# Performance work log

Hardware: AMD Instinct MI355X
Metric: run time of the kernel (lower is better)

The kernel has to match this reference:

```python
import jax, jax.numpy as jnp
import numpy as np

B, S, H = 1, 1024, 2048
I = 1408            # moe_intermediate_size
E = 16              # n_routed_experts
TOP_K = 4           # num_experts_per_tok
N_GROUP = 4
TOPK_GROUP = 2
N_SHARED = 2
SCALE = 2.5         # routed_scaling_factor
SI = I * N_SHARED   # shared expert intermediate size


def setup_inputs() -> dict:
    key = jax.random.key(0)
    ks = jax.random.split(key, 9)
    s = 0.02
    return {
        "hidden_states": jax.random.normal(ks[0], (B, S, H), jnp.float32),
        "gate_w": jax.random.normal(ks[1], (E, H), jnp.float32) * s,
        "gate_bias": jnp.zeros((E,), jnp.float32),
        "w_gate": jax.random.normal(ks[2], (E, I, H), jnp.float32) * s,
        "w_up": jax.random.normal(ks[3], (E, I, H), jnp.float32) * s,
        "w_down": jax.random.normal(ks[4], (E, H, I), jnp.float32) * s,
        "sw_gate": jax.random.normal(ks[5], (SI, H), jnp.float32) * s,
        "sw_up": jax.random.normal(ks[6], (SI, H), jnp.float32) * s,
        "sw_down": jax.random.normal(ks[7], (H, SI), jnp.float32) * s,
    }


def _gate(x, gate_w, gate_bias):
    # x: [T, H] -> combine weights [T, E]
    T = x.shape[0]
    logits = x @ gate_w.T                                  # [T, E]
    scores = jax.nn.sigmoid(logits) + gate_bias            # [T, E]
    gsz = E // N_GROUP
    group_scores = scores.reshape(T, N_GROUP, gsz).max(-1)  # [T, G]
    _, sel_groups = jax.lax.top_k(group_scores, TOPK_GROUP)  # [T, kg]
    gmask = jnp.zeros((T, N_GROUP), scores.dtype).at[
        jnp.arange(T)[:, None], sel_groups].set(1.0)        # [T, G]
    mask = jnp.repeat(gmask, gsz, axis=1)                   # [T, E]
    masked = scores * mask
    w, idx = jax.lax.top_k(masked, TOP_K)                   # [T, k]
    w = w / (w.sum(-1, keepdims=True) + 1e-6)
    combine = jnp.zeros((T, E), w.dtype).at[
        jnp.arange(T)[:, None], idx].add(w)                 # [T, E]
    return combine


def reference(hidden_states, gate_w, gate_bias, w_gate, w_up, w_down,
              sw_gate, sw_up, sw_down):
    x = hidden_states.reshape(-1, H)                        # [T, H]
    combine = _gate(x, gate_w, gate_bias)                   # [T, E]
    # dense dispatch: every expert sees all tokens; zero combine weight
    # for unrouted tokens reproduces the masked gather/scatter loop exactly
    g = jnp.einsum('th,eih->tei', x, w_gate)
    u = jnp.einsum('th,eih->tei', x, w_up)
    h = jax.nn.silu(g) * u                                   # [T, E, I]
    y = jnp.einsum('tei,ehi->teh', h, w_down)                # [T, E, H]
    routed = jnp.einsum('te,teh->th', combine, y) * SCALE    # [T, H]
    # shared experts (one wide MLP)
    shared = (jax.nn.silu(x @ sw_gate.T) * (x @ sw_up.T)) @ sw_down.T
    return (routed + shared).reshape(B, S, H)
```

## Files before the change

### kernel.cpp

```cpp
#include <hip/hip_runtime.h>
#include <hip/hip_bf16.h>

#define TTOK  1024
#define HDIM  2048
#define IDIM  1408
#define NEXP  16
#define SIDIM 2816
#define RSCALE 2.5f

typedef __bf16 bf16_t;
typedef bf16_t bf16x8 __attribute__((ext_vector_type(8)));
typedef float  f32x4  __attribute__((ext_vector_type(4)));

static const size_t OFF_XBF   = 0;
static const size_t OFF_HBUF  = 4194304;
static const size_t OFF_SHBUF = OFF_HBUF + 17301504;
static const size_t OFF_TOPKI = OFF_SHBUF + 5767168;
static const size_t OFF_TOPKW = OFF_TOPKI + 16384;
static const size_t OFF_TOKL  = OFF_TOPKW + 16384;
static const size_t OFF_WGTL  = OFF_TOKL + 24576;
static const size_t OFF_CNT   = OFF_WGTL + 24576;
static const size_t OFF_POFF  = OFF_CNT + 256;

union Pack4 { bf16_t b[4]; unsigned long long u64; };

__device__ __forceinline__ f32x4 mfma16(bf16x8 a, bf16x8 b, f32x4 c) {
    return __builtin_amdgcn_mfma_f32_16x16x32_bf16(a, b, c, 0, 0, 0);
}
__device__ __forceinline__ bf16x8 frag_read(const bf16_t* lds, int row, int slot) {
    int sw = slot ^ (row & 7);
    return *(const bf16x8*)(lds + row * 64 + sw * 8);
}

__global__ __launch_bounds__(256) void k_convert(const float* __restrict__ x,
                                                 bf16_t* __restrict__ xb, int n) {
    int i = (blockIdx.x * 256 + threadIdx.x) * 4;
    if (i < n) {
        float4 v = *(const float4*)(x + i);
        Pack4 p;
        p.b[0] = (bf16_t)v.x; p.b[1] = (bf16_t)v.y;
        p.b[2] = (bf16_t)v.z; p.b[3] = (bf16_t)v.w;
        *(unsigned long long*)(xb + i) = p.u64;
    }
}

__global__ __launch_bounds__(256) void k_gate(const float* __restrict__ x,
                                              const float* __restrict__ gw,
                                              const float* __restrict__ gb,
                                              int* __restrict__ topki,
                                              float* __restrict__ topkw,
                                              int* __restrict__ counts) {
    int t = blockIdx.x;
    int tid = threadIdx.x;
    int e = tid >> 4, li = tid & 15;
    const float* xr = x + (size_t)t * HDIM;
    const float* wr = gw + (size_t)e * HDIM;
    float s = 0.f;
#pragma unroll
    for (int j = 0; j < 32; ++j) {
        int off = (j * 16 + li) * 4;
        float4 a = *(const float4*)(xr + off);
        float4 b = *(const float4*)(wr + off);
        s += a.x * b.x + a.y * b.y + a.z * b.z + a.w * b.w;
    }
    __shared__ float red[16][16];
    __shared__ float scores[16];
    red[e][li] = s;
    __syncthreads();
    if (tid < 16) {
        float acc = 0.f;
#pragma unroll
        for (int j = 0; j < 16; ++j) acc += red[tid][j];
        scores[tid] = 1.f / (1.f + expf(-acc)) + gb[tid];
    }
    __syncthreads();
    if (tid == 0) {
        float gsc[4];
#pragma unroll
        for (int g = 0; g < 4; ++g) {
            float m = scores[g * 4];
            for (int j = 1; j < 4; ++j) m = fmaxf(m, scores[g * 4 + j]);
            gsc[g] = m;
        }
        bool gsel[4] = {false, false, false, false};
        for (int k = 0; k < 2; ++k) {
            int best = 0; float bv = -1e30f;
            for (int g = 0; g < 4; ++g)
                if (!gsel[g] && gsc[g] > bv) { bv = gsc[g]; best = g; }
            gsel[best] = true;
        }
        float msc[16];
        for (int i = 0; i < 16; ++i) msc[i] = gsel[i >> 2] ? scores[i] : -1.f;
        int bidx[4]; float bw[4]; float wsum = 0.f;
        for (int k = 0; k < 4; ++k) {
            int best = 0; float bv = -2e30f;
            for (int i = 0; i < 16; ++i)
                if (msc[i] > bv) { bv = msc[i]; best = i; }
            msc[best] = -3e30f;
            bidx[k] = best; bw[k] = bv; wsum += bv;
        }
        float inv = 1.f / (wsum + 1e-6f);
        for (int k = 0; k < 4; ++k) {
            topki[t * 4 + k] = bidx[k];
            topkw[t * 4 + k] = bw[k] * inv * RSCALE;
            atomicAdd(&counts[bidx[k]], 1);
        }
    }
}

__global__ void k_scan(const int* __restrict__ counts, int* __restrict__ poff) {
    if (threadIdx.x == 0 && blockIdx.x == 0) {
        int acc = 0;
        for (int e = 0; e < NEXP; ++e) {
            poff[e] = acc;
            acc += (counts[e] + 127) & ~127;
        }
    }
}

__global__ __launch_bounds__(64) void k_compact(const int* __restrict__ topki,
                                                const float* __restrict__ topkw,
                                                const int* __restrict__ counts,
                                                const int* __restrict__ poff,
                                                int* __restrict__ tokl,
                                                float* __restrict__ wgtl) {
    int e = blockIdx.x;
    int lane = threadIdx.x;
    int base = poff[e];
    int cur = 0;
    for (int t0 = 0; t0 < TTOK; t0 += 64) {
        int t = t0 + lane;
        int4   idx = *(const int4*)(topki + t * 4);
        float4 wv  = *(const float4*)(topkw + t * 4);
        bool has = false; float w = 0.f;
        if      (idx.x == e) { has = true; w = wv.x; }
        else if (idx.y == e) { has = true; w = wv.y; }
        else if (idx.z == e) { has = true; w = wv.z; }
        else if (idx.w == e) { has = true; w = wv.w; }
        unsigned long long b = __ballot(has);
        int pos = cur + __popcll(b & ((1ull << lane) - 1ull));
        if (has) { tokl[base + pos] = t; wgtl[base + pos] = w; }
        cur += __popcll(b);
    }
    int padded = (counts[e] + 127) & ~127;
    for (int i = cur + lane; i < padded; i += 64) {
        tokl[base + i] = -1; wgtl[base + i] = 0.f;
    }
}

__global__ __launch_bounds__(256, 2) void k_mlp1_routed(
        const bf16_t* __restrict__ xb, const float* __restrict__ wg,
        const float* __restrict__ wu, const int* __restrict__ counts,
        const int* __restrict__ poff, const int* __restrict__ tokl,
        bf16_t* __restrict__ hbuf) {
    int bid = blockIdx.x;
    int e = bid / 88, rem = bid % 88;
    int mt = rem / 11, nt = rem % 11;
    int cnt = counts[e];
    if (mt * 128 >= cnt) return;
    int rowbase = poff[e] + mt * 128;
    const float* wgp = wg + (size_t)e * IDIM * HDIM + (size_t)(nt * 128) * HDIM;
    const float* wup = wu + (size_t)e * IDIM * HDIM + (size_t)(nt * 128) * HDIM;

    __shared__ bf16_t aL[128 * 64];
    __shared__ bf16_t gL[128 * 64];
    __shared__ bf16_t uL[128 * 64];

    int tid = threadIdx.x;
    int lane = tid & 63;
    int wid = tid >> 6;
    int wm = wid >> 1, wn = wid & 1;

    f32x4 accg[4][4], accu[4][4];
#pragma unroll
    for (int m = 0; m < 4; ++m)
#pragma unroll
        for (int n = 0; n < 4; ++n) {
            accg[m][n] = (f32x4){0.f, 0.f, 0.f, 0.f};
            accu[m][n] = (f32x4){0.f, 0.f, 0.f, 0.f};
        }

    int arow_ = tid >> 3, alane = tid & 7;
    int brow_ = tid >> 4, blane = tid & 15;
    int atok[4];
#pragma unroll
    for (int p = 0; p < 4; ++p) atok[p] = tokl[rowbase + p * 32 + arow_];

    for (int kt = 0; kt < HDIM / 64; ++kt) {
#pragma unroll
        for (int p = 0; p < 4; ++p) {
            int r = p * 32 + arow_;
            uint4 v = make_uint4(0, 0, 0, 0);
            int tok = atok[p];
            if (tok >= 0)
                v = *(const uint4*)(xb + (size_t)tok * HDIM + kt * 64 + alane * 8);
            int sw = alane ^ (r & 7);
            *(uint4*)(aL + r * 64 + sw * 8) = v;
        }
#pragma unroll
        for (int p = 0; p < 8; ++p) {
            int r = p * 16 + brow_;
            const float* sg = wgp + (size_t)r * HDIM + kt * 64 + blane * 4;
            const float* su = wup + (size_t)r * HDIM + kt * 64 + blane * 4;
            float4 vg = *(const float4*)sg;
            float4 vu = *(const float4*)su;
            int sw = (blane >> 1) ^ (r & 7);
            int half = blane & 1;
            Pack4 pg, pu;
            pg.b[0] = (bf16_t)vg.x; pg.b[1] = (bf16_t)vg.y;
            pg.b[2] = (bf16_t)vg.z; pg.b[3] = (bf16_t)vg.w;
            pu.b[0] = (bf16_t)vu.x; pu.b[1] = (bf16_t)vu.y;
            pu.b[2] = (bf16_t)vu.z; pu.b[3] = (bf16_t)vu.w;
            *(unsigned long long*)(gL + r * 64 + sw * 8 + half * 4) = pg.u64;
            *(unsigned long long*)(uL + r * 64 + sw * 8 + half * 4) = pu.u64;
        }
        __syncthreads();
#pragma unroll
        for (int ks = 0; ks < 2; ++ks) {
            bf16x8 af[4], bg[4], bu[4];
            int slot = ks * 4 + (lane >> 4);
#pragma unroll
            for (int m = 0; m < 4; ++m)
                af[m] = frag_read(aL, wm * 64 + m * 16 + (lane & 15), slot);
#pragma unroll
            for (int n = 0; n < 4; ++n) {
                bg[n] = frag_read(gL, wn * 64 + n * 16 + (lane & 15), slot);
                bu[n] = frag_read(uL, wn * 64 + n * 16 + (lane & 15), slot);
            }
#pragma unroll
            for (int m = 0; m < 4; ++m)
#pragma unroll
                for (int n = 0; n < 4; ++n) {
                    accg[m][n] = mfma16(af[m], bg[n], accg[m][n]);
                    accu[m][n] = mfma16(af[m], bu[n], accu[m][n]);
                }
        }
        __syncthreads();
    }
    int col0 = nt * 128 + wn * 64 + (lane & 15);
#pragma unroll
    for (int m = 0; m < 4; ++m) {
        int rloc = wm * 64 + m * 16 + ((lane >> 4) << 2);
#pragma unroll
        for (int ri = 0; ri < 4; ++ri) {
            bf16_t* dst = hbuf + (size_t)(rowbase + rloc + ri) * IDIM + col0;
#pragma unroll
            for (int n = 0; n < 4; ++n) {
                float g = accg[m][n][ri], u = accu[m][n][ri];
                float h = g / (1.f + __expf(-g)) * u;
                dst[n * 16] = (bf16_t)h;
            }
        }
    }
}

__global__ __launch_bounds__(256, 2) void k_mlp1_shared(
        const bf16_t* __restrict__ xb, const float* __restrict__ swg,
        const float* __restrict__ swu, bf16_t* __restrict__ shbuf) {
    int bid = blockIdx.x;
    int mt = bid / 22, nt = bid % 22;
    int rowbase = mt * 128;
    const float* wgp = swg + (size_t)(nt * 128) * HDIM;
    const float* wup = swu + (size_t)(nt * 128) * HDIM;

    __shared__ bf16_t aL[128 * 64];
    __shared__ bf16_t gL[128 * 64];
    __shared__ bf16_t uL[128 * 64];

    int tid = threadIdx.x;
    int lane = tid & 63;
    int wid = tid >> 6;
    int wm = wid >> 1, wn = wid & 1;

    f32x4 accg[4][4], accu[4][4];
#pragma unroll
    for (int m = 0; m < 4; ++m)
#pragma unroll
        for (int n = 0; n < 4; ++n) {
            accg[m][n] = (f32x4){0.f, 0.f, 0.f, 0.f};
            accu[m][n] = (f32x4){0.f, 0.f, 0.f, 0.f};
        }
    int arow_ = tid >> 3, alane = tid & 7;
    int brow_ = tid >> 4, blane = tid & 15;

    for (int kt = 0; kt < HDIM / 64; ++kt) {
#pragma unroll
        for (int p = 0; p < 4; ++p) {
            int r = p * 32 + arow_;
            uint4 v = *(const uint4*)(xb + (size_t)(rowbase + r) * HDIM + kt * 64 + alane * 8);
            int sw = alane ^ (r & 7);
            *(uint4*)(aL + r * 64 + sw * 8) = v;
        }
#pragma unroll
        for (int p = 0; p < 8; ++p) {
            int r = p * 16 + brow_;
            float4 vg = *(const float4*)(wgp + (size_t)r * HDIM + kt * 64 + blane * 4);
            float4 vu = *(const float4*)(wup + (size_t)r * HDIM + kt * 64 + blane * 4);
            int sw = (blane >> 1) ^ (r & 7);
            int half = blane & 1;
            Pack4 pg, pu;
            pg.b[0] = (bf16_t)vg.x; pg.b[1] = (bf16_t)vg.y;
            pg.b[2] = (bf16_t)vg.z; pg.b[3] = (bf16_t)vg.w;
            pu.b[0] = (bf16_t)vu.x; pu.b[1] = (bf16_t)vu.y;
            pu.b[2] = (bf16_t)vu.z; pu.b[3] = (bf16_t)vu.w;
            *(unsigned long long*)(gL + r * 64 + sw * 8 + half * 4) = pg.u64;
            *(unsigned long long*)(uL + r * 64 + sw * 8 + half * 4) = pu.u64;
        }
        __syncthreads();
#pragma unroll
        for (int ks = 0; ks < 2; ++ks) {
            bf16x8 af[4], bg[4], bu[4];
            int slot = ks * 4 + (lane >> 4);
#pragma unroll
            for (int m = 0; m < 4; ++m)
                af[m] = frag_read(aL, wm * 64 + m * 16 + (lane & 15), slot);
#pragma unroll
            for (int n = 0; n < 4; ++n) {
                bg[n] = frag_read(gL, wn * 64 + n * 16 + (lane & 15), slot);
                bu[n] = frag_read(uL, wn * 64 + n * 16 + (lane & 15), slot);
            }
#pragma unroll
            for (int m = 0; m < 4; ++m)
#pragma unroll
                for (int n = 0; n < 4; ++n) {
                    accg[m][n] = mfma16(af[m], bg[n], accg[m][n]);
                    accu[m][n] = mfma16(af[m], bu[n], accu[m][n]);
                }
        }
        __syncthreads();
    }
    int col0 = nt * 128 + wn * 64 + (lane & 15);
#pragma unroll
    for (int m = 0; m < 4; ++m) {
        int rloc = wm * 64 + m * 16 + ((lane >> 4) << 2);
#pragma unroll
        for (int ri = 0; ri < 4; ++ri) {
            bf16_t* dst = shbuf + (size_t)(rowbase + rloc + ri) * SIDIM + col0;
#pragma unroll
            for (int n = 0; n < 4; ++n) {
                float g = accg[m][n][ri], u = accu[m][n][ri];
                float h = g / (1.f + __expf(-g)) * u;
                dst[n * 16] = (bf16_t)h;
            }
        }
    }
}

__global__ __launch_bounds__(256, 2) void k_down_shared(
        const bf16_t* __restrict__ shbuf, const float* __restrict__ swd,
        float* __restrict__ out) {
    int bid = blockIdx.x;
    int mt = bid >> 4, nt = bid & 15;
    int rowbase = mt * 128;
    const float* wp = swd + (size_t)(nt * 128) * SIDIM;

    __shared__ bf16_t aL[128 * 64];
    __shared__ bf16_t bL[128 * 64];

    int tid = threadIdx.x;
    int lane = tid & 63;
    int wid = tid >> 6;
    int wm = wid >> 1, wn = wid & 1;

    f32x4 acc[4][4];
#pragma unroll
    for (int m = 0; m < 4; ++m)
#pragma unroll
        for (int n = 0; n < 4; ++n) acc[m][n] = (f32x4){0.f, 0.f, 0.f, 0.f};

    int arow_ = tid >> 3, alane = tid & 7;
    int brow_ = tid >> 4, blane = tid & 15;

    for (int kt = 0; kt < SIDIM / 64; ++kt) {
#pragma unroll
        for (int p = 0; p < 4; ++p) {
            int r = p * 32 + arow_;
            uint4 v = *(const uint4*)(shbuf + (size_t)(rowbase + r) * SIDIM + kt * 64 + alane * 8);
            int sw = alane ^ (r & 7);
            *(uint4*)(aL + r * 64 + sw * 8) = v;
        }
#pragma unroll
        for (int p = 0; p < 8; ++p) {
            int r = p * 16 + brow_;
            float4 v = *(const float4*)(wp + (size_t)r * SIDIM + kt * 64 + blane * 4);
            int sw = (blane >> 1) ^ (r & 7);
            int half = blane & 1;
            Pack4 pb;
            pb.b[0] = (bf16_t)v.x; pb.b[1] = (bf16_t)v.y;
            pb.b[2] = (bf16_t)v.z; pb.b[3] = (bf16_t)v.w;
            *(unsigned long long*)(bL + r * 64 + sw * 8 + half * 4) = pb.u64;
        }
        __syncthreads();
#pragma unroll
        for (int ks = 0; ks < 2; ++ks) {
            bf16x8 af[4], bf[4];
            int slot = ks * 4 + (lane >> 4);
#pragma unroll
            for (int m = 0; m < 4; ++m)
                af[m] = frag_read(aL, wm * 64 + m * 16 + (lane & 15), slot);
#pragma unroll
            for (int n = 0; n < 4; ++n)
                bf[n] = frag_read(bL, wn * 64 + n * 16 + (lane & 15), slot);
#pragma unroll
            for (int m = 0; m < 4; ++m)
#pragma unroll
                for (int n = 0; n < 4; ++n)
                    acc[m][n] = mfma16(af[m], bf[n], acc[m][n]);
        }
        __syncthreads();
    }
    int col0 = nt * 128 + wn * 64 + (lane & 15);
#pragma unroll
    for (int m = 0; m < 4; ++m) {
        int rloc = wm * 64 + m * 16 + ((lane >> 4) << 2);
#pragma unroll
        for (int ri = 0; ri < 4; ++ri) {
            float* dst = out + (size_t)(rowbase + rloc + ri) * HDIM + col0;
#pragma unroll
            for (int n = 0; n < 4; ++n) dst[n * 16] = acc[m][n][ri];
        }
    }
}

__global__ __launch_bounds__(256, 2) void k_down_routed(
        const bf16_t* __restrict__ hbuf, const float* __restrict__ wd,
        const int* __restrict__ counts, const int* __restrict__ poff,
        const int* __restrict__ tokl, const float* __restrict__ wgtl,
        float* __restrict__ out) {
    int bid = blockIdx.x;
    int e = bid >> 7, rem = bid & 127;
    int mt = rem >> 4, nt = rem & 15;
    int cnt = counts[e];
    if (mt * 128 >= cnt) return;
    int rowbase = poff[e] + mt * 128;
    const float* wp = wd + (size_t)e * HDIM * IDIM + (size_t)(nt * 128) * IDIM;

    __shared__ bf16_t aL[128 * 64];
    __shared__ bf16_t bL[128 * 64];

    int tid = threadIdx.x;
    int lane = tid & 63;
    int wid = tid >> 6;
    int wm = wid >> 1, wn = wid & 1;

    f32x4 acc[4][4];
#pragma unroll
    for (int m = 0; m < 4; ++m)
#pragma unroll
        for (int n = 0; n < 4; ++n) acc[m][n] = (f32x4){0.f, 0.f, 0.f, 0.f};

    int arow_ = tid >> 3, alane = tid & 7;
    int brow_ = tid >> 4, blane = tid & 15;

    for (int kt = 0; kt < IDIM / 64; ++kt) {
#pragma unroll
        for (int p = 0; p < 4; ++p) {
            int r = p * 32 + arow_;
            uint4 v = *(const uint4*)(hbuf + (size_t)(rowbase + r) * IDIM + kt * 64 + alane * 8);
            int sw = alane ^ (r & 7);
            *(uint4*)(aL + r * 64 + sw * 8) = v;
        }
#pragma unroll
        for (int p = 0; p < 8; ++p) {
            int r = p * 16 + brow_;
            float4 v = *(const float4*)(wp + (size_t)r * IDIM + kt * 64 + blane * 4);
            int sw = (blane >> 1) ^ (r & 7);
            int half = blane & 1;
            Pack4 pb;
            pb.b[0] = (bf16_t)v.x; pb.b[1] = (bf16_t)v.y;
            pb.b[2] = (bf16_t)v.z; pb.b[3] = (bf16_t)v.w;
            *(unsigned long long*)(bL + r * 64 + sw * 8 + half * 4) = pb.u64;
        }
        __syncthreads();
#pragma unroll
        for (int ks = 0; ks < 2; ++ks) {
            bf16x8 af[4], bf[4];
            int slot = ks * 4 + (lane >> 4);
#pragma unroll
            for (int m = 0; m < 4; ++m)
                af[m] = frag_read(aL, wm * 64 + m * 16 + (lane & 15), slot);
#pragma unroll
            for (int n = 0; n < 4; ++n)
                bf[n] = frag_read(bL, wn * 64 + n * 16 + (lane & 15), slot);
#pragma unroll
            for (int m = 0; m < 4; ++m)
#pragma unroll
                for (int n = 0; n < 4; ++n)
                    acc[m][n] = mfma16(af[m], bf[n], acc[m][n]);
        }
        __syncthreads();
    }
    int col0 = nt * 128 + wn * 64 + (lane & 15);
#pragma unroll
    for (int m = 0; m < 4; ++m) {
        int rloc = wm * 64 + m * 16 + ((lane >> 4) << 2);
#pragma unroll
        for (int ri = 0; ri < 4; ++ri) {
            int row = rowbase + rloc + ri;
            int tok = tokl[row];
            if (tok < 0) continue;
            float wgt = wgtl[row];
            float* dst = out + (size_t)tok * HDIM + col0;
#pragma unroll
            for (int n = 0; n < 4; ++n)
                atomicAdd(dst + n * 16, wgt * acc[m][n][ri]);
        }
    }
}

extern "C" void kernel_launch(void* const* d_in, const int* in_sizes, int n_in,
                              void* d_out, int out_size, void* d_ws, size_t ws_size,
                              hipStream_t stream) {
    const float* x       = (const float*)d_in[0];
    const float* gate_w  = (const float*)d_in[1];
    const float* gate_b  = (const float*)d_in[2];
    const float* w_gate  = (const float*)d_in[3];
    const float* w_up    = (const float*)d_in[4];
    const float* w_down  = (const float*)d_in[5];
    const float* sw_gate = (const float*)d_in[6];
    const float* sw_up   = (const float*)d_in[7];
    const float* sw_down = (const float*)d_in[8];
    float* out = (float*)d_out;

    char* ws = (char*)d_ws;
    bf16_t* xb    = (bf16_t*)(ws + OFF_XBF);
    bf16_t* hbuf  = (bf16_t*)(ws + OFF_HBUF);
    bf16_t* shbuf = (bf16_t*)(ws + OFF_SHBUF);
    int*    topki = (int*)(ws + OFF_TOPKI);
    float*  topkw = (float*)(ws + OFF_TOPKW);
    int*    tokl  = (int*)(ws + OFF_TOKL);
    float*  wgtl  = (float*)(ws + OFF_WGTL);
    int*    counts= (int*)(ws + OFF_CNT);
    int*    poff  = (int*)(ws + OFF_POFF);

    hipMemsetAsync(counts, 0, 64, stream);
    k_convert<<<2048, 256, 0, stream>>>(x, xb, TTOK * HDIM);
    k_gate<<<TTOK, 256, 0, stream>>>(x, gate_w, gate_b, topki, topkw, counts);
    k_scan<<<1, 64, 0, stream>>>(counts, poff);
    k_compact<<<NEXP, 64, 0, stream>>>(topki, topkw, counts, poff, tokl, wgtl);
    k_mlp1_routed<<<NEXP * 8 * 11, 256, 0, stream>>>(xb, w_gate, w_up, counts, poff, tokl, hbuf);
    k_mlp1_shared<<<8 * 22, 256, 0, stream>>>(xb, sw_gate, sw_up, shbuf);
    k_down_shared<<<8 * 16, 256, 0, stream>>>(shbuf, sw_down, out);
    k_down_routed<<<NEXP * 8 * 16, 256, 0, stream>>>(hbuf, w_down, counts, poff, tokl, wgtl, out);
}
```

Measured before the change: 0.9997 ms.

## Merge routed/shared MLP kernels, halve N tile, prefetch next K tile, swizzle XCDs

Routed and shared expert GEMMs are merged into one launch for the up/gate stage and one for the down stage. The N tile shrinks from 128 to 64, which doubles the block count and lowers register and LDS use, so occupancy can be raised to 3 blocks per CU in the down kernel. Global loads for the next K tile are issued into registers before the MFMA loop (register double-buffering), and a block-index swizzle groups neighbouring tiles onto the same XCD to improve L2 reuse. The shared down projection now uses atomics into a zeroed output, which adds a memset, and narrower tiles re-read the activations more often.

```diff
diff --git a/kernel.cpp b/kernel.cpp
--- a/kernel.cpp
+++ b/kernel.cpp
@@ -30,6 +30,10 @@
 __device__ __forceinline__ bf16x8 frag_read(const bf16_t* lds, int row, int slot) {
     int sw = slot ^ (row & 7);
     return *(const bf16x8*)(lds + row * 64 + sw * 8);
+}
+__device__ __forceinline__ int xcd_swz(int bid, int grid) {
+    int q = grid >> 3;
+    return (bid & 7) * q + (bid >> 3);
 }
 
 __global__ __launch_bounds__(256) void k_convert(const float* __restrict__ x,
@@ -148,104 +152,134 @@
     }
 }
 
-__global__ __launch_bounds__(256, 2) void k_mlp1_routed(
-        const bf16_t* __restrict__ xb, const float* __restrict__ wg,
-        const float* __restrict__ wu, const int* __restrict__ counts,
-        const int* __restrict__ poff, const int* __restrict__ tokl,
-        bf16_t* __restrict__ hbuf) {
-    int bid = blockIdx.x;
-    int e = bid / 88, rem = bid % 88;
-    int mt = rem / 11, nt = rem % 11;
-    int cnt = counts[e];
-    if (mt * 128 >= cnt) return;
-    int rowbase = poff[e] + mt * 128;
-    const float* wgp = wg + (size_t)e * IDIM * HDIM + (size_t)(nt * 128) * HDIM;
-    const float* wup = wu + (size_t)e * IDIM * HDIM + (size_t)(nt * 128) * HDIM;
+#define GRID_MLP1 (NEXP * 22 * 8 + 44 * 8)
+
+__global__ __launch_bounds__(256, 2) void k_mlp1(
+        const bf16_t* __restrict__ xb,
+        const float* __restrict__ wg, const float* __restrict__ wu,
+        const float* __restrict__ swg, const float* __restrict__ swu,
+        const int* __restrict__ counts, const int* __restrict__ poff,
+        const int* __restrict__ tokl,
+        bf16_t* __restrict__ hbuf, bf16_t* __restrict__ shbuf) {
+    int bid = xcd_swz(blockIdx.x, GRID_MLP1);
+    bool routed = bid < NEXP * 22 * 8;
+    const float *wgp, *wup;
+    bf16_t* outp;
+    int old_, rowbase, ntcol;
+    if (routed) {
+        int e = bid / 176, rem = bid % 176;
+        int nt = rem / 8, mt = rem % 8;
+        if (mt * 128 >= counts[e]) return;
+        rowbase = poff[e] + mt * 128;
+        size_t wo = (size_t)e * IDIM * HDIM + (size_t)(nt * 64) * HDIM;
+        wgp = wg + wo; wup = wu + wo;
+        outp = hbuf; old_ = IDIM; ntcol = nt * 64;
+    } else {
+        int sb = bid - NEXP * 22 * 8;
+        int nt = sb / 8, mt = sb % 8;
+        rowbase = mt * 128;
+        size_t wo = (size_t)(nt * 64) * HDIM;
+        wgp = swg + wo; wup = swu + wo;
+        outp = shbuf; old_ = SIDIM; ntcol = nt * 64;
+    }
 
     __shared__ bf16_t aL[128 * 64];
-    __shared__ bf16_t gL[128 * 64];
-    __shared__ bf16_t uL[128 * 64];
-
-    int tid = threadIdx.x;
-    int lane = tid & 63;
-    int wid = tid >> 6;
+    __shared__ bf16_t gL[64 * 64];
+    __shared__ bf16_t uL[64 * 64];
+
+    int tid = threadIdx.x, lane = tid & 63, wid = tid >> 6;
     int wm = wid >> 1, wn = wid & 1;
-
-    f32x4 accg[4][4], accu[4][4];
+    int arow_ = tid >> 3, alane = tid & 7;
+    int brow_ = tid >> 4, blane = tid & 15;
+
+    int tokA[4];
+#pragma unroll
+    for (int p = 0; p < 4; ++p) {
+        int r = rowbase + p * 32 + arow_;
+        int tk = routed ? tokl[r] : r;
+        tokA[p] = tk < 0 ? 0 : tk;
+    }
+
+    f32x4 accg[4][2], accu[4][2];
 #pragma unroll
     for (int m = 0; m < 4; ++m)
 #pragma unroll
-        for (int n = 0; n < 4; ++n) {
+        for (int n = 0; n < 2; ++n) {
             accg[m][n] = (f32x4){0.f, 0.f, 0.f, 0.f};
             accu[m][n] = (f32x4){0.f, 0.f, 0.f, 0.f};
         }
 
-    int arow_ = tid >> 3, alane = tid & 7;
-    int brow_ = tid >> 4, blane = tid & 15;
-    int atok[4];
-#pragma unroll
-    for (int p = 0; p < 4; ++p) atok[p] = tokl[rowbase + p * 32 + arow_];
+    uint4  sa[4];
+    float4 sg[4], su[4];
+
+#define MLP1_LOAD(KT) do {                                                        \
+    _Pragma("unroll")                                                             \
+    for (int p = 0; p < 4; ++p)                                                   \
+        sa[p] = *(const uint4*)(xb + (size_t)tokA[p] * HDIM + (KT) * 64 + alane * 8); \
+    _Pragma("unroll")                                                             \
+    for (int p = 0; p < 4; ++p) {                                                 \
+        size_t off = (size_t)(p * 16 + brow_) * HDIM + (KT) * 64 + blane * 4;     \
+        sg[p] = *(const float4*)(wgp + off);                                      \
+        su[p] = *(const float4*)(wup + off);                                      \
+    }                                                                             \
+} while (0)
+
+    MLP1_LOAD(0);
 
     for (int kt = 0; kt < HDIM / 64; ++kt) {
 #pragma unroll
         for (int p = 0; p < 4; ++p) {
             int r = p * 32 + arow_;
-            uint4 v = make_uint4(0, 0, 0, 0);
-            int tok = atok[p];
-            if (tok >= 0)
-                v = *(const uint4*)(xb + (size_t)tok * HDIM + kt * 64 + alane * 8);
-            int sw = alane ^ (r & 7);
-            *(uint4*)(aL + r * 64 + sw * 8) = v;
-        }
-#pragma unroll
-        for (int p = 0; p < 8; ++p) {
+            *(uint4*)(aL + r * 64 + (alane ^ (r & 7)) * 8) = sa[p];
+        }
+#pragma unroll
+        for (int p = 0; p < 4; ++p) {
             int r = p * 16 + brow_;
-            const float* sg = wgp + (size_t)r * HDIM + kt * 64 + blane * 4;
-            const float* su = wup + (size_t)r * HDIM + kt * 64 + blane * 4;
-            float4 vg = *(const float4*)sg;
-            float4 vu = *(const float4*)su;
-            int sw = (blane >> 1) ^ (r & 7);
-            int half = blane & 1;
+            int sw = (blane >> 1) ^ (r & 7), half = blane & 1;
             Pack4 pg, pu;
-            pg.b[0] = (bf16_t)vg.x; pg.b[1] = (bf16_t)vg.y;
-            pg.b[2] = (bf16_t)vg.z; pg.b[3] = (bf16_t)vg.w;
-            pu.b[0] = (bf16_t)vu.x; pu.b[1] = (bf16_t)vu.y;
-            pu.b[2] = (bf16_t)vu.z; pu.b[3] = (bf16_t)vu.w;
+            pg.b[0] = (bf16_t)sg[p].x; pg.b[1] = (bf16_t)sg[p].y;
+            pg.b[2] = (bf16_t)sg[p].z; pg.b[3] = (bf16_t)sg[p].w;
+            pu.b[0] = (bf16_t)su[p].x; pu.b[1] = (bf16_t)su[p].y;
+            pu.b[2] = (bf16_t)su[p].z; pu.b[3] = (bf16_t)su[p].w;
             *(unsigned long long*)(gL + r * 64 + sw * 8 + half * 4) = pg.u64;
             *(unsigned long long*)(uL + r * 64 + sw * 8 + half * 4) = pu.u64;
         }
         __syncthreads();
+        int ktn = (kt + 1 < HDIM / 64) ? kt + 1 : kt;
+        MLP1_LOAD(ktn);
 #pragma unroll
         for (int ks = 0; ks < 2; ++ks) {
-            bf16x8 af[4], bg[4], bu[4];
+            bf16x8 af[4], bg[2], bu[2];
             int slot = ks * 4 + (lane >> 4);
 #pragma unroll
             for (int m = 0; m < 4; ++m)
                 af[m] = frag_read(aL, wm * 64 + m * 16 + (lane & 15), slot);
 #pragma unroll
-            for (int n = 0; n < 4; ++n) {
-                bg[n] = frag_read(gL, wn * 64 + n * 16 + (lane & 15), slot);
-                bu[n] = frag_read(uL, wn * 64 + n * 16 + (lane & 15), slot);
+            for (int n = 0; n < 2; ++n) {
+                bg[n] = frag_read(gL, wn * 32 + n * 16 + (lane & 15), slot);
+                bu[n] = frag_read(uL, wn * 32 + n * 16 + (lane & 15), slot);
             }
 #pragma unroll
             for (int m = 0; m < 4; ++m)
 #pragma unroll
-                for (int n = 0; n < 4; ++n) {
+                for (int n = 0; n < 2; ++n) {
                     accg[m][n] = mfma16(af[m], bg[n], accg[m][n]);
                     accu[m][n] = mfma16(af[m], bu[n], accu[m][n]);
                 }
         }
         __syncthreads();
     }
-    int col0 = nt * 128 + wn * 64 + (lane & 15);
+#undef MLP1_LOAD
+
+    int col0 = ntcol + wn * 32 + (lane & 15);
 #pragma unroll
     for (int m = 0; m < 4; ++m) {
         int rloc = wm * 64 + m * 16 + ((lane >> 4) << 2);
 #pragma unroll
         for (int ri = 0; ri < 4; ++ri) {
-            bf16_t* dst = hbuf + (size_t)(rowbase + rloc + ri) * IDIM + col0;
-#pragma unroll
-            for (int n = 0; n < 4; ++n) {
+            bf16_t* dst = outp + (size_t)(rowbase + rloc + ri) * old_ + col0;
+#pragma unroll
+            for (int n = 0; n < 2; ++n) {
                 float g = accg[m][n][ri], u = accu[m][n][ri];
                 float h = g / (1.f + __expf(-g)) * u;
                 dst[n * 16] = (bf16_t)h;
@@ -254,255 +288,124 @@
     }
 }
 
-__global__ __launch_bounds__(256, 2) void k_mlp1_shared(
-        const bf16_t* __restrict__ xb, const float* __restrict__ swg,
-        const float* __restrict__ swu, bf16_t* __restrict__ shbuf) {
-    int bid = blockIdx.x;
-    int mt = bid / 22, nt = bid % 22;
-    int rowbase = mt * 128;
-    const float* wgp = swg + (size_t)(nt * 128) * HDIM;
-    const float* wup = swu + (size_t)(nt * 128) * HDIM;
-
-    __shared__ bf16_t aL[128 * 64];
-    __shared__ bf16_t gL[128 * 64];
-    __shared__ bf16_t uL[128 * 64];
-
-    int tid = threadIdx.x;
-    int lane = tid & 63;
-    int wid = tid >> 6;
-    int wm = wid >> 1, wn = wid & 1;
-
-    f32x4 accg[4][4], accu[4][4];
-#pragma unroll
-    for (int m = 0; m < 4; ++m)
-#pragma unroll
-        for (int n = 0; n < 4; ++n) {
-            accg[m][n] = (f32x4){0.f, 0.f, 0.f, 0.f};
-            accu[m][n] = (f32x4){0.f, 0.f, 0.f, 0.f};
-        }
-    int arow_ = tid >> 3, alane = tid & 7;
-    int brow_ = tid >> 4, blane = tid & 15;
-
-    for (int kt = 0; kt < HDIM / 64; ++kt) {
-#pragma unroll
-        for (int p = 0; p < 4; ++p) {
-            int r = p * 32 + arow_;
-            uint4 v = *(const uint4*)(xb + (size_t)(rowbase + r) * HDIM + kt * 64 + alane * 8);
-            int sw = alane ^ (r & 7);
-            *(uint4*)(aL + r * 64 + sw * 8) = v;
-        }
-#pragma unroll
-        for (int p = 0; p < 8; ++p) {
-            int r = p * 16 + brow_;
-            float4 vg = *(const float4*)(wgp + (size_t)r * HDIM + kt * 64 + blane * 4);
-            float4 vu = *(const float4*)(wup + (size_t)r * HDIM + kt * 64 + blane * 4);
-            int sw = (blane >> 1) ^ (r & 7);
-            int half = blane & 1;
-            Pack4 pg, pu;
-            pg.b[0] = (bf16_t)vg.x; pg.b[1] = (bf16_t)vg.y;
-            pg.b[2] = (bf16_t)vg.z; pg.b[3] = (bf16_t)vg.w;
-            pu.b[0] = (bf16_t)vu.x; pu.b[1] = (bf16_t)vu.y;
-            pu.b[2] = (bf16_t)vu.z; pu.b[3] = (bf16_t)vu.w;
-            *(unsigned long long*)(gL + r * 64 + sw * 8 + half * 4) = pg.u64;
-            *(unsigned long long*)(uL + r * 64 + sw * 8 + half * 4) = pu.u64;
-        }
-        __syncthreads();
-#pragma unroll
-        for (int ks = 0; ks < 2; ++ks) {
-            bf16x8 af[4], bg[4], bu[4];
-            int slot = ks * 4 + (lane >> 4);
-#pragma unroll
-            for (int m = 0; m < 4; ++m)
-                af[m] = frag_read(aL, wm * 64 + m * 16 + (lane & 15), slot);
-#pragma unroll
-            for (int n = 0; n < 4; ++n) {
-                bg[n] = frag_read(gL, wn * 64 + n * 16 + (lane & 15), slot);
-                bu[n] = frag_read(uL, wn * 64 + n * 16 + (lane & 15), slot);
-            }
-#pragma unroll
-            for (int m = 0; m < 4; ++m)
-#pragma unroll
-                for (int n = 0; n < 4; ++n) {
-                    accg[m][n] = mfma16(af[m], bg[n], accg[m][n]);
-                    accu[m][n] = mfma16(af[m], bu[n], accu[m][n]);
-                }
-        }
-        __syncthreads();
-    }
-    int col0 = nt * 128 + wn * 64 + (lane & 15);
-#pragma unroll
-    for (int m = 0; m < 4; ++m) {
-        int rloc = wm * 64 + m * 16 + ((lane >> 4) << 2);
-#pragma unroll
-        for (int ri = 0; ri < 4; ++ri) {
-            bf16_t* dst = shbuf + (size_t)(rowbase + rloc + ri) * SIDIM + col0;
-#pragma unroll
-            for (int n = 0; n < 4; ++n) {
-                float g = accg[m][n][ri], u = accu[m][n][ri];
-                float h = g / (1.f + __expf(-g)) * u;
-                dst[n * 16] = (bf16_t)h;
-            }
-        }
-    }
-}
-
-__global__ __launch_bounds__(256, 2) void k_down_shared(
-        const bf16_t* __restrict__ shbuf, const float* __restrict__ swd,
-        float* __restrict__ out) {
-    int bid = blockIdx.x;
-    int mt = bid >> 4, nt = bid & 15;
-    int rowbase = mt * 128;
-    const float* wp = swd + (size_t)(nt * 128) * SIDIM;
-
-    __shared__ bf16_t aL[128 * 64];
-    __shared__ bf16_t bL[128 * 64];
-
-    int tid = threadIdx.x;
-    int lane = tid & 63;
-    int wid = tid >> 6;
-    int wm = wid >> 1, wn = wid & 1;
-
-    f32x4 acc[4][4];
-#pragma unroll
-    for (int m = 0; m < 4; ++m)
-#pragma unroll
-        for (int n = 0; n < 4; ++n) acc[m][n] = (f32x4){0.f, 0.f, 0.f, 0.f};
-
-    int arow_ = tid >> 3, alane = tid & 7;
-    int brow_ = tid >> 4, blane = tid & 15;
-
-    for (int kt = 0; kt < SIDIM / 64; ++kt) {
-#pragma unroll
-        for (int p = 0; p < 4; ++p) {
-            int r = p * 32 + arow_;
-            uint4 v = *(const uint4*)(shbuf + (size_t)(rowbase + r) * SIDIM + kt * 64 + alane * 8);
-            int sw = alane ^ (r & 7);
-            *(uint4*)(aL + r * 64 + sw * 8) = v;
-        }
-#pragma unroll
-        for (int p = 0; p < 8; ++p) {
-            int r = p * 16 + brow_;
-            float4 v = *(const float4*)(wp + (size_t)r * SIDIM + kt * 64 + blane * 4);
-            int sw = (blane >> 1) ^ (r & 7);
-            int half = blane & 1;
-            Pack4 pb;
-            pb.b[0] = (bf16_t)v.x; pb.b[1] = (bf16_t)v.y;
-            pb.b[2] = (bf16_t)v.z; pb.b[3] = (bf16_t)v.w;
-            *(unsigned long long*)(bL + r * 64 + sw * 8 + half * 4) = pb.u64;
-        }
-        __syncthreads();
-#pragma unroll
-        for (int ks = 0; ks < 2; ++ks) {
-            bf16x8 af[4], bf[4];
-            int slot = ks * 4 + (lane >> 4);
-#pragma unroll
-            for (int m = 0; m < 4; ++m)
-                af[m] = frag_read(aL, wm * 64 + m * 16 + (lane & 15), slot);
-#pragma unroll
-            for (int n = 0; n < 4; ++n)
-                bf[n] = frag_read(bL, wn * 64 + n * 16 + (lane & 15), slot);
-#pragma unroll
-            for (int m = 0; m < 4; ++m)
-#pragma unroll
-                for (int n = 0; n < 4; ++n)
-                    acc[m][n] = mfma16(af[m], bf[n], acc[m][n]);
-        }
-        __syncthreads();
-    }
-    int col0 = nt * 128 + wn * 64 + (lane & 15);
-#pragma unroll
-    for (int m = 0; m < 4; ++m) {
-        int rloc = wm * 64 + m * 16 + ((lane >> 4) << 2);
-#pragma unroll
-        for (int ri = 0; ri < 4; ++ri) {
-            float* dst = out + (size_t)(rowbase + rloc + ri) * HDIM + col0;
-#pragma unroll
-            for (int n = 0; n < 4; ++n) dst[n * 16] = acc[m][n][ri];
-        }
-    }
-}
-
-__global__ __launch_bounds__(256, 2) void k_down_routed(
-        const bf16_t* __restrict__ hbuf, const float* __restrict__ wd,
+#define GRID_DOWN (NEXP * 32 * 8 + 32 * 8)
+
+__global__ __launch_bounds__(256, 3) void k_down(
+        const bf16_t* __restrict__ hbuf, const bf16_t* __restrict__ shbuf,
+        const float* __restrict__ wd, const float* __restrict__ swd,
         const int* __restrict__ counts, const int* __restrict__ poff,
         const int* __restrict__ tokl, const float* __restrict__ wgtl,
         float* __restrict__ out) {
-    int bid = blockIdx.x;
-    int e = bid >> 7, rem = bid & 127;
-    int mt = rem >> 4, nt = rem & 15;
-    int cnt = counts[e];
-    if (mt * 128 >= cnt) return;
-    int rowbase = poff[e] + mt * 128;
-    const float* wp = wd + (size_t)e * HDIM * IDIM + (size_t)(nt * 128) * IDIM;
+    int bid = xcd_swz(blockIdx.x, GRID_DOWN);
+    bool routed = bid < NEXP * 32 * 8;
+    const bf16_t* ap;
+    const float* bp;
+    int ald, nkt, rowbase, ntcol;
+    if (routed) {
+        int e = bid / 256, rem = bid % 256;
+        int nt = rem / 8, mt = rem % 8;
+        if (mt * 128 >= counts[e]) return;
+        rowbase = poff[e] + mt * 128;
+        ap = hbuf; ald = IDIM; nkt = IDIM / 64;
+        bp = wd + (size_t)e * HDIM * IDIM + (size_t)(nt * 64) * IDIM;
+        ntcol = nt * 64;
+    } else {
+        int sb = bid - NEXP * 32 * 8;
+        int nt = sb / 8, mt = sb % 8;
+        rowbase = mt * 128;
+        ap = shbuf; ald = SIDIM; nkt = SIDIM / 64;
+        bp = swd + (size_t)(nt * 64) * SIDIM;
+        ntcol = nt * 64;
+    }
 
     __shared__ bf16_t aL[128 * 64];
-    __shared__ bf16_t bL[128 * 64];
-
-    int tid = threadIdx.x;
-    int lane = tid & 63;
-    int wid = tid >> 6;
+    __shared__ bf16_t bL[64 * 64];
+
+    int tid = threadIdx.x, lane = tid & 63, wid = tid >> 6;
     int wm = wid >> 1, wn = wid & 1;
-
-    f32x4 acc[4][4];
-#pragma unroll
-    for (int m = 0; m < 4; ++m)
-#pragma unroll
-        for (int n = 0; n < 4; ++n) acc[m][n] = (f32x4){0.f, 0.f, 0.f, 0.f};
-
     int arow_ = tid >> 3, alane = tid & 7;
     int brow_ = tid >> 4, blane = tid & 15;
 
-    for (int kt = 0; kt < IDIM / 64; ++kt) {
+    f32x4 acc[4][2];
+#pragma unroll
+    for (int m = 0; m < 4; ++m)
+#pragma unroll
+        for (int n = 0; n < 2; ++n) acc[m][n] = (f32x4){0.f, 0.f, 0.f, 0.f};
+
+    uint4  sa[4];
+    float4 sb[4];
+
+#define DOWN_LOAD(KT) do {                                                            \
+    _Pragma("unroll")                                                                 \
+    for (int p = 0; p < 4; ++p)                                                       \
+        sa[p] = *(const uint4*)(ap + (size_t)(rowbase + p * 32 + arow_) * ald +       \
+                                (KT) * 64 + alane * 8);                               \
+    _Pragma("unroll")                                                                 \
+    for (int p = 0; p < 4; ++p)                                                       \
+        sb[p] = *(const float4*)(bp + (size_t)(p * 16 + brow_) * ald +                \
+                                 (KT) * 64 + blane * 4);                              \
+} while (0)
+
+    DOWN_LOAD(0);
+
+    for (int kt = 0; kt < nkt; ++kt) {
 #pragma unroll
         for (int p = 0; p < 4; ++p) {
             int r = p * 32 + arow_;
-            uint4 v = *(const uint4*)(hbuf + (size_t)(rowbase + r) * IDIM + kt * 64 + alane * 8);
-            int sw = alane ^ (r & 7);
-            *(uint4*)(aL + r * 64 + sw * 8) = v;
-        }
-#pragma unroll
-        for (int p = 0; p < 8; ++p) {
+            *(uint4*)(aL + r * 64 + (alane ^ (r & 7)) * 8) = sa[p];
+        }
+#pragma unroll
+        for (int p = 0; p < 4; ++p) {
             int r = p * 16 + brow_;
-            float4 v = *(const float4*)(wp + (size_t)r * IDIM + kt * 64 + blane * 4);
-            int sw = (blane >> 1) ^ (r & 7);
-            int half = blane & 1;
+            int sw = (blane >> 1) ^ (r & 7), half = blane & 1;
             Pack4 pb;
-            pb.b[0] = (bf16_t)v.x; pb.b[1] = (bf16_t)v.y;
-            pb.b[2] = (bf16_t)v.z; pb.b[3] = (bf16_t)v.w;
+            pb.b[0] = (bf16_t)sb[p].x; pb.b[1] = (bf16_t)sb[p].y;
+            pb.b[2] = (bf16_t)sb[p].z; pb.b[3] = (bf16_t)sb[p].w;
             *(unsigned long long*)(bL + r * 64 + sw * 8 + half * 4) = pb.u64;
         }
         __syncthreads();
+        int ktn = (kt + 1 < nkt) ? kt + 1 : kt;
+        DOWN_LOAD(ktn);
 #pragma unroll
         for (int ks = 0; ks < 2; ++ks) {
-            bf16x8 af[4], bf[4];
+            bf16x8 af[4], bf[2];
             int slot = ks * 4 + (lane >> 4);
 #pragma unroll
             for (int m = 0; m < 4; ++m)
                 af[m] = frag_read(aL, wm * 64 + m * 16 + (lane & 15), slot);
 #pragma unroll
-            for (int n = 0; n < 4; ++n)
-                bf[n] = frag_read(bL, wn * 64 + n * 16 + (lane & 15), slot);
+            for (int n = 0; n < 2; ++n)
+                bf[n] = frag_read(bL, wn * 32 + n * 16 + (lane & 15), slot);
 #pragma unroll
             for (int m = 0; m < 4; ++m)
 #pragma unroll
-                for (int n = 0; n < 4; ++n)
+                for (int n = 0; n < 2; ++n)
                     acc[m][n] = mfma16(af[m], bf[n], acc[m][n]);
         }
         __syncthreads();
     }
-    int col0 = nt * 128 + wn * 64 + (lane & 15);
+#undef DOWN_LOAD
+
+    int col0 = ntcol + wn * 32 + (lane & 15);
 #pragma unroll
     for (int m = 0; m < 4; ++m) {
         int rloc = wm * 64 + m * 16 + ((lane >> 4) << 2);
 #pragma unroll
         for (int ri = 0; ri < 4; ++ri) {
             int row = rowbase + rloc + ri;
-            int tok = tokl[row];
-            if (tok < 0) continue;
-            float wgt = wgtl[row];
-            float* dst = out + (size_t)tok * HDIM + col0;
-#pragma unroll
-            for (int n = 0; n < 4; ++n)
+            float* dst;
+            float wgt;
+            if (routed) {
+                int tok = tokl[row];
+                if (tok < 0) continue;
+                wgt = wgtl[row];
+                dst = out + (size_t)tok * HDIM + col0;
+            } else {
+                wgt = 1.f;
+                dst = out + (size_t)row * HDIM + col0;
+            }
+#pragma unroll
+            for (int n = 0; n < 2; ++n)
                 atomicAdd(dst + n * 16, wgt * acc[m][n][ri]);
         }
     }
@@ -534,12 +437,13 @@
     int*    poff  = (int*)(ws + OFF_POFF);
 
     hipMemsetAsync(counts, 0, 64, stream);
+    hipMemsetAsync(out, 0, (size_t)TTOK * HDIM * sizeof(float), stream);
     k_convert<<<2048, 256, 0, stream>>>(x, xb, TTOK * HDIM);
     k_gate<<<TTOK, 256, 0, stream>>>(x, gate_w, gate_b, topki, topkw, counts);
     k_scan<<<1, 64, 0, stream>>>(counts, poff);
     k_compact<<<NEXP, 64, 0, stream>>>(topki, topkw, counts, poff, tokl, wgtl);
-    k_mlp1_routed<<<NEXP * 8 * 11, 256, 0, stream>>>(xb, w_gate, w_up, counts, poff, tokl, hbuf);
-    k_mlp1_shared<<<8 * 22, 256, 0, stream>>>(xb, sw_gate, sw_up, shbuf);
-    k_down_shared<<<8 * 16, 256, 0, stream>>>(shbuf, sw_down, out);
-    k_down_routed<<<NEXP * 8 * 16, 256, 0, stream>>>(hbuf, w_down, counts, poff, tokl, wgtl, out);
-}
+    k_mlp1<<<GRID_MLP1, 256, 0, stream>>>(xb, w_gate, w_up, sw_gate, sw_up,
+                                          counts, poff, tokl, hbuf, shbuf);
+    k_down<<<GRID_DOWN, 256, 0, stream>>>(hbuf, shbuf, w_down, sw_down,
+                                          counts, poff, tokl, wgtl, out);
+}
```

New measurement: 1.651 ms. +65.1%, slower.
